# Kernel tuning notes

Measured on AMD Instinct MI355X. Metric: run time of the kernel, lower is better.

The kernel has to match this reference:

```python
import jax, jax.numpy as jnp
import numpy as np

N, M, K, D = 2048, 2048, 8, 64
BLUR, SCALING = 0.05, 0.8
EPS_MIN = BLUR ** 2            # geomloss: eps = blur^p, p=2
DIAM2 = 16.0                   # static diameter^2 estimate for jit-static eps schedule
NEG = -1e9                     # log-weight for masked-out points


def _eps_schedule():
    eps, e = [], DIAM2
    while e > EPS_MIN:
        eps.append(e)
        e *= SCALING ** 2      # geomloss multiplies eps by scaling^p per step
    eps.append(EPS_MIN)
    return jnp.asarray(eps, jnp.float32)


def _softmin(eps, C, h):
    # -eps * logsumexp_j( h_j - C_ij/eps );  C:[n,m], h:[m] (h = log_w + pot/eps)
    return -eps * jax.nn.logsumexp(h[None, :] - C / eps, axis=1)


def _sq_cost(u, v):
    # geomloss p=2 cost: ||u-v||^2 / 2
    d2 = jnp.sum(u * u, 1)[:, None] + jnp.sum(v * v, 1)[None, :] - 2.0 * (u @ v.T)
    return 0.5 * jnp.maximum(d2, 0.0)


def _sinkhorn_divergence(Cxy, Cxx, Cyy, log_a, log_b, a, b, eps_arr):
    # debiased sinkhorn divergence S = <a, f-f_aa> + <b, g-g_bb>, eps-scaling,
    # symmetric (averaged) updates; loop is detached, one differentiable
    # extrapolation step at eps_min (geomloss-style envelope gradient).
    Cxy_s, Cxx_s, Cyy_s = (jax.lax.stop_gradient(c) for c in (Cxy, Cxx, Cyy))
    n, m = Cxy.shape

    def step(carry, eps):
        f_ab, g_ab, f_aa, g_bb = carry
        ft = _softmin(eps, Cxy_s, log_b + g_ab / eps)
        gt = _softmin(eps, Cxy_s.T, log_a + f_ab / eps)
        f_aa = 0.5 * (f_aa + _softmin(eps, Cxx_s, log_a + f_aa / eps))
        g_bb = 0.5 * (g_bb + _softmin(eps, Cyy_s, log_b + g_bb / eps))
        return (0.5 * (f_ab + ft), 0.5 * (g_ab + gt), f_aa, g_bb), None

    init = (jnp.zeros(n, jnp.float32), jnp.zeros(m, jnp.float32),
            jnp.zeros(n, jnp.float32), jnp.zeros(m, jnp.float32))
    (f_ab, g_ab, f_aa, g_bb), _ = jax.lax.scan(step, init, eps_arr)
    f_ab, g_ab, f_aa, g_bb = (jax.lax.stop_gradient(p) for p in (f_ab, g_ab, f_aa, g_bb))

    eps = eps_arr[-1]
    f = _softmin(eps, Cxy, log_b + g_ab / eps)
    g = _softmin(eps, Cxy.T, log_a + f_ab / eps)
    faa = _softmin(eps, Cxx, log_a + f_aa / eps)
    gbb = _softmin(eps, Cyy, log_b + g_bb / eps)
    return jnp.sum(a * (f - faa)) + jnp.sum(b * (g - gbb))


def setup_inputs() -> dict:
    key = jax.random.key(0)
    k1, k2, k3, k4, k5 = jax.random.split(key, 5)
    return {
        "x": jax.random.normal(k1, (N, D), jnp.float32),
        "cluster_centers": jax.random.normal(k2, (K, D), jnp.float32),
        "filling_target": jax.random.uniform(k3, (K,), jnp.float32),
        "target": jax.random.normal(k4, (M, D), jnp.float32),
        "prediction": jax.random.randint(k5, (M,), 0, K, jnp.int64),
    }


def reference(x, cluster_centers, filling_target, target, prediction):
    # kmeans_predict: nearest center assignment
    d2c = jnp.sum((x[:, None, :] - cluster_centers[None, :, :]) ** 2, axis=-1)  # [N,K]
    pred_x = jnp.argmin(d2c, axis=1)                                            # [N]

    ks = jnp.arange(K)
    mx = (pred_x[None, :] == ks[:, None]).astype(jnp.float32)       # [K,N]
    my = (prediction[None, :] == ks[:, None]).astype(jnp.float32)   # [K,M]
    cnt_x, cnt_y = mx.sum(1), my.sum(1)

    # compute_cluster_filling_mse: cluster occupancy fraction vs target
    loss_fil = jnp.mean((cnt_x / N - filling_target) ** 2)

    a = mx / jnp.maximum(cnt_x, 1.0)[:, None]
    b = my / jnp.maximum(cnt_y, 1.0)[:, None]
    log_a = jnp.where(mx > 0, -jnp.log(jnp.maximum(cnt_x, 1.0))[:, None], NEG)
    log_b = jnp.where(my > 0, -jnp.log(jnp.maximum(cnt_y, 1.0))[:, None], NEG)
    valid = (cnt_x > 0.5) & (cnt_y > 0.5)

    # shared dense cost matrices (cluster structure enters only via weights)
    Cxy, Cxx, Cyy = _sq_cost(x, target), _sq_cost(x, x), _sq_cost(target, target)
    eps_arr = _eps_schedule()
    div = jax.vmap(lambda la, lb, aa, bb: _sinkhorn_divergence(
        Cxy, Cxx, Cyy, la, lb, aa, bb, eps_arr))(log_a, log_b, a, b)   # [K]

    loss_med = jnp.sum(jnp.where(valid, div, 0.0))
    return loss_fil + loss_med
```

## Files before the change

kernel.cpp:

```cpp
#include <hip/hip_runtime.h>

#define NN 2048
#define MM 2048
#define KC 8
#define DD 64
#define PN (NN + 4*KC + 32)
#define PM (MM + 4*KC + 32)
#define TOTROWS (2*(NN+MM))
#define CPAD (2*NN*MM + NN*NN + MM*MM + 6*(NN+MM) + 256)
#define PADV 3.0e38f
#define LN2F    0.6931471805599453f
#define INVLN2F 1.4426950408889634f

struct Params {
  const float* x; const float* centers; const float* ftarg;
  const float* y; const int* predy;
  float* out;
  int* zr;
  int* pred_x;
  int* cntx; int* cnty; int* off_x; int* off_y; int* pox; int* poy;
  int* bxy; int* byx; int* bxx; int* byy;
  int* tpre;
  float* la; float* lb; int* valid; float* acc;
  float* Xp; float* Yp; float* xn; float* yn;
  float* Fab; float* Faa; float* Gab; float* Gbb;
  int4* meta;
  float* fin;
  int* dsti;
  float* Call;
};

__device__ __forceinline__ float wredmax(float v){
  #pragma unroll
  for(int m=32;m>=1;m>>=1) v = fmaxf(v, __shfl_xor(v,m,64));
  return v;
}
__device__ __forceinline__ float wredsum(float v){
  #pragma unroll
  for(int m=32;m>=1;m>>=1) v += __shfl_xor(v,m,64);
  return v;
}

__global__ void __launch_bounds__(256) k_pred(Params p){
  const int gtid = blockIdx.x*blockDim.x + threadIdx.x;
  const int nth  = gridDim.x*blockDim.x;

  for(int i=gtid;i<2*PN;i+=nth){ p.Fab[i]=0.f; p.Faa[i]=0.f; }
  for(int j=gtid;j<2*PM;j+=nth){ p.Gab[j]=0.f; p.Gbb[j]=0.f; }

  for(int i=gtid;i<NN;i+=nth){
    const float4* xi = (const float4*)(p.x + i*DD);
    float best = 3.4e38f; int bk = 0;
    for(int k=0;k<KC;k++){
      const float4* ck = (const float4*)(p.centers + k*DD);
      float s = 0.f;
      #pragma unroll
      for(int q=0;q<DD/4;q++){ float4 a=xi[q], b=ck[q];
        float dx=a.x-b.x, dy=a.y-b.y, dz=a.z-b.z, dw=a.w-b.w;
        s += dx*dx+dy*dy+dz*dz+dw*dw; }
      if(s < best){ best = s; bk = k; }
    }
    p.pred_x[i] = bk;
    atomicAdd(&p.zr[8+bk], 1);
  }
  for(int j=gtid;j<MM;j+=nth) atomicAdd(&p.zr[16 + p.predy[j]], 1);
}

__global__ void __launch_bounds__(256) k_pack(Params p){
  __shared__ int scx[KC], scy[KC];
  __shared__ int sox[KC+1], soy[KC+1], spx[KC], spy[KC];
  __shared__ int sbxy[KC], sbyx[KC], sbxx[KC], sbyy[KC], sval[KC];
  __shared__ float sla[KC], slb[KC];
  const int tid = threadIdx.x;
  const int gtid = blockIdx.x*blockDim.x + tid;
  const int nth  = gridDim.x*blockDim.x;

  if(tid==0){
    int ox=0, oy=0, px=0, py=0; float lf=0.f;
    for(int k=0;k<KC;k++){
      int nk=p.zr[8+k], mk=p.zr[16+k];
      scx[k]=nk; scy[k]=mk;
      sox[k]=ox; soy[k]=oy; spx[k]=px; spy[k]=py;
      ox+=nk; oy+=mk; px=(px+nk+3)&~3; py=(py+mk+3)&~3;
      sla[k] = -logf(fmaxf((float)nk,1.f));
      slb[k] = -logf(fmaxf((float)mk,1.f));
      sval[k] = (nk>0 && mk>0)?1:0;
      float df = (float)nk/(float)NN - p.ftarg[k];
      lf += df*df;
    }
    sox[KC]=ox; soy[KC]=oy;
    int run=0;
    for(int k=0;k<KC;k++){ int nk=scx[k], mk=scy[k]; sbxy[k]=run; run+=nk*((mk+3)&~3); }
    for(int k=0;k<KC;k++){ int nk=scx[k], mk=scy[k]; sbyx[k]=run; run+=mk*((nk+3)&~3); }
    for(int k=0;k<KC;k++){ int nk=scx[k];            sbxx[k]=run; run+=nk*((nk+3)&~3); }
    for(int k=0;k<KC;k++){ int mk=scy[k];            sbyy[k]=run; run+=mk*((mk+3)&~3); }
    if(blockIdx.x==0){
      for(int k=0;k<KC;k++){
        p.cntx[k]=scx[k]; p.cnty[k]=scy[k];
        p.off_x[k]=sox[k]; p.off_y[k]=soy[k];
        p.pox[k]=spx[k]; p.poy[k]=spy[k];
        p.bxy[k]=sbxy[k]; p.byx[k]=sbyx[k]; p.bxx[k]=sbxx[k]; p.byy[k]=sbyy[k];
        p.la[k]=sla[k]; p.lb[k]=slb[k]; p.valid[k]=sval[k];
      }
      int trun=0;
      for(int e=0;e<32;e++){
        int seg=e>>3, k=e&7;
        int nk=scx[k], mk=scy[k];
        int nrows = (seg==0)?nk:(seg==1)?mk:(seg==2)?nk:mk;
        int rs    = (seg==0)?((mk+3)&~3):(seg==1)?((nk+3)&~3):(seg==2)?((nk+3)&~3):((mk+3)&~3);
        p.tpre[e]=trun;
        trun += ((nrows+63)>>6) * ((rs+63)>>6);
      }
      p.tpre[32]=trun;
      *p.acc = lf/(float)KC;
    }
  }
  __syncthreads();

  for(int i=gtid;i<NN;i+=nth){
    int k=p.pred_x[i];
    int pos = sox[k] + atomicAdd(&p.zr[24+k],1);
    const float4* xi=(const float4*)(p.x+i*DD);
    float4* dst=(float4*)(p.Xp+(size_t)pos*DD);
    float s=0.f;
    #pragma unroll
    for(int q=0;q<DD/4;q++){ float4 v=xi[q]; dst[q]=v;
      s += v.x*v.x+v.y*v.y+v.z*v.z+v.w*v.w; }
    p.xn[pos]=s;
  }
  for(int j=gtid;j<MM;j+=nth){
    int k=p.predy[j];
    int pos = soy[k] + atomicAdd(&p.zr[32+k],1);
    const float4* yj=(const float4*)(p.y+j*DD);
    float4* dst=(float4*)(p.Yp+(size_t)pos*DD);
    float s=0.f;
    #pragma unroll
    for(int q=0;q<DD/4;q++){ float4 v=yj[q]; dst[q]=v;
      s += v.x*v.x+v.y*v.y+v.z*v.z+v.w*v.w; }
    p.yn[pos]=s;
  }

  for(int row=gtid; row<TOTROWS; row+=nth){
    int grp = (row>=NN) + (row>=NN+MM) + (row>=2*NN+MM);
    int pidx = row - ((grp==0)?0:(grp==1)?NN:(grp==2)?(NN+MM):(2*NN+MM));
    const int* offs = (grp==0||grp==2)? sox : soy;
    int k=0;
    #pragma unroll
    for(int q=1;q<KC;q++) if(pidx>=offs[q]) k=q;
    int r = pidx - offs[k];
    int nk=scx[k], mk=scy[k];
    int rsx=(nk+3)&~3, rsy=(mk+3)&~3;
    int coff, rs, di; float hc, fv; int hoff;
    if(grp==0){ rs=rsy; coff=sbxy[k]+r*rs; hoff=spy[k]; hc=slb[k]; di=spx[k]+r;
      fv = sval[k] ?  1.f/(float)nk : 0.f; }
    else if(grp==1){ rs=rsx; coff=sbyx[k]+r*rs; hoff=spx[k]; hc=sla[k]; di=spy[k]+r;
      fv = sval[k] ?  1.f/(float)mk : 0.f; }
    else if(grp==2){ rs=rsx; coff=sbxx[k]+r*rs; hoff=spx[k]; hc=sla[k]; di=spx[k]+r;
      fv = sval[k] ? -1.f/(float)nk : 0.f; }
    else { rs=rsy; coff=sbyy[k]+r*rs; hoff=spy[k]; hc=slb[k]; di=spy[k]+r;
      fv = sval[k] ? -1.f/(float)mk : 0.f; }
    p.meta[row] = make_int4(coff, hoff, rs, __float_as_int(hc*INVLN2F));
    p.fin[row]  = fv;
    p.dsti[row] = di;
  }
}

__global__ void __launch_bounds__(256) k4_cost(Params p){
  __shared__ float As[64*68];
  __shared__ float Bt[64*68];
  const int tid = threadIdx.x;
  const int T = p.tpre[32];

  for(int tile=blockIdx.x; tile<T; tile+=gridDim.x){
    int e=0;
    for(int q=1;q<32;q++) if(tile>=p.tpre[q]) e=q;
    int seg=e>>3, k=e&7;
    int nk=p.cntx[k], mk=p.cnty[k];
    int rsx=(nk+3)&~3, rsy=(mk+3)&~3;
    const float *Apts, *Bpts, *nA, *nB; int nrows, ncol, rs, base;
    if(seg==0){ Apts=p.Xp+(size_t)p.off_x[k]*DD; Bpts=p.Yp+(size_t)p.off_y[k]*DD;
      nA=p.xn+p.off_x[k]; nB=p.yn+p.off_y[k]; nrows=nk; ncol=mk; rs=rsy; base=p.bxy[k]; }
    else if(seg==1){ Apts=p.Yp+(size_t)p.off_y[k]*DD; Bpts=p.Xp+(size_t)p.off_x[k]*DD;
      nA=p.yn+p.off_y[k]; nB=p.xn+p.off_x[k]; nrows=mk; ncol=nk; rs=rsx; base=p.byx[k]; }
    else if(seg==2){ Apts=p.Xp+(size_t)p.off_x[k]*DD; Bpts=Apts;
      nA=p.xn+p.off_x[k]; nB=nA; nrows=nk; ncol=nk; rs=rsx; base=p.bxx[k]; }
    else { Apts=p.Yp+(size_t)p.off_y[k]*DD; Bpts=Apts;
      nA=p.yn+p.off_y[k]; nB=nA; nrows=mk; ncol=mk; rs=rsy; base=p.byy[k]; }
    int ntc=(rs+63)>>6;
    int lt = tile - p.tpre[e];
    int tr = lt/ntc, tc = lt - tr*ntc;

    __syncthreads();
    for(int l=tid;l<1024;l+=256){
      int row=l>>4, c4=l&15;
      int gA=tr*64+row;
      float4 va = (gA<nrows)? ((const float4*)Apts)[gA*16+c4] : make_float4(0.f,0.f,0.f,0.f);
      *(float4*)&As[row*68 + c4*4] = va;
      int gB=tc*64+row;
      float4 vb = (gB<ncol)? ((const float4*)Bpts)[gB*16+c4] : make_float4(0.f,0.f,0.f,0.f);
      Bt[(c4*4+0)*68+row]=vb.x; Bt[(c4*4+1)*68+row]=vb.y;
      Bt[(c4*4+2)*68+row]=vb.z; Bt[(c4*4+3)*68+row]=vb.w;
    }
    __syncthreads();

    int tx=tid&15, ty=tid>>4;
    float4 acc[4] = {make_float4(0,0,0,0),make_float4(0,0,0,0),
                     make_float4(0,0,0,0),make_float4(0,0,0,0)};
    for(int kk=0;kk<64;kk+=4){
      float4 a0=*(float4*)&As[(ty*4+0)*68+kk];
      float4 a1=*(float4*)&As[(ty*4+1)*68+kk];
      float4 a2=*(float4*)&As[(ty*4+2)*68+kk];
      float4 a3=*(float4*)&As[(ty*4+3)*68+kk];
      float4 b0=*(float4*)&Bt[(kk+0)*68+tx*4];
      float4 b1=*(float4*)&Bt[(kk+1)*68+tx*4];
      float4 b2=*(float4*)&Bt[(kk+2)*68+tx*4];
      float4 b3=*(float4*)&Bt[(kk+3)*68+tx*4];
      #define ACCROW(i,AI) \
        acc[i].x = fmaf(AI.x,b0.x, fmaf(AI.y,b1.x, fmaf(AI.z,b2.x, fmaf(AI.w,b3.x, acc[i].x)))); \
        acc[i].y = fmaf(AI.x,b0.y, fmaf(AI.y,b1.y, fmaf(AI.z,b2.y, fmaf(AI.w,b3.y, acc[i].y)))); \
        acc[i].z = fmaf(AI.x,b0.z, fmaf(AI.y,b1.z, fmaf(AI.z,b2.z, fmaf(AI.w,b3.z, acc[i].z)))); \
        acc[i].w = fmaf(AI.x,b0.w, fmaf(AI.y,b1.w, fmaf(AI.w,b3.w, fmaf(AI.z,b2.w, acc[i].w))));
      ACCROW(0,a0) ACCROW(1,a1) ACCROW(2,a2) ACCROW(3,a3)
      #undef ACCROW
    }

    int gc0 = tc*64 + tx*4;
    #pragma unroll
    for(int i=0;i<4;i++){
      int gr = tr*64 + ty*4 + i;
      if(gr >= nrows) continue;
      float xr = nA[gr];
      float v[4]; float d[4]={acc[i].x,acc[i].y,acc[i].z,acc[i].w};
      #pragma unroll
      for(int j=0;j<4;j++){
        int gc = gc0+j;
        v[j] = PADV;
        if(gc < ncol) v[j] = 0.5f*fmaxf(xr + nB[gc] - 2.f*d[j], 0.f);
      }
      if(gc0+3 < rs){
        *(float4*)&p.Call[(size_t)base + (size_t)gr*rs + gc0] = make_float4(v[0],v[1],v[2],v[3]);
      } else {
        for(int j=0;j<4;j++) if(gc0+j < rs) p.Call[(size_t)base + (size_t)gr*rs + gc0+j] = v[j];
      }
    }
  }
}

__global__ void __launch_bounds__(256) k_iter(Params p, float eps, int cur){
  const int w = blockIdx.x*4 + (threadIdx.x>>6);
  const int lane = threadIdx.x & 63;
  const int r0 = w*2, r1 = r0+1;
  const int grp = (r0>=NN) + (r0>=NN+MM) + (r0>=2*NN+MM);
  const float* po; float* fam; int famN;
  if(grp==0){ po=p.Gab+cur*PM; fam=p.Fab; famN=PN; }
  else if(grp==1){ po=p.Fab+cur*PN; fam=p.Gab; famN=PM; }
  else if(grp==2){ po=p.Faa+cur*PN; fam=p.Faa; famN=PN; }
  else { po=p.Gbb+cur*PM; fam=p.Gbb; famN=PM; }

  int4 m0 = p.meta[r0], m1 = p.meta[r1];
  const float* C0=p.Call+m0.x; const float* P0=po+m0.y; float h0=__int_as_float(m0.w);
  const float* C1=p.Call+m1.x; const float* P1=po+m1.y; float h1=__int_as_float(m1.w);
  const int rs0=m0.z, rs1=m1.z, rsm = rs0>rs1?rs0:rs1;
  const float s1 = (1.0f/eps)*INVLN2F;

  float mA=-3.4e38f,sA=0.f,mB=-3.4e38f,sB=0.f;
  for(int c0=lane*4; c0<rsm; c0+=256){
    if(c0<rs0){
      float4 cv=*(const float4*)(C0+c0), pv=*(const float4*)(P0+c0);
      float w0=fmaf(pv.x-cv.x,s1,h0), w1=fmaf(pv.y-cv.y,s1,h0);
      float w2=fmaf(pv.z-cv.z,s1,h0), w3=fmaf(pv.w-cv.w,s1,h0);
      float lm=fmaxf(fmaxf(w0,w1),fmaxf(w2,w3));
      float mn=fmaxf(mA,lm);
      sA = sA*exp2f(mA-mn) + (exp2f(w0-mn)+exp2f(w1-mn)) + (exp2f(w2-mn)+exp2f(w3-mn));
      mA = mn;
    }
    if(c0<rs1){
      float4 cv=*(const float4*)(C1+c0), pv=*(const float4*)(P1+c0);
      float w0=fmaf(pv.x-cv.x,s1,h1), w1=fmaf(pv.y-cv.y,s1,h1);
      float w2=fmaf(pv.z-cv.z,s1,h1), w3=fmaf(pv.w-cv.w,s1,h1);
      float lm=fmaxf(fmaxf(w0,w1),fmaxf(w2,w3));
      float mn=fmaxf(mB,lm);
      sB = sB*exp2f(mB-mn) + (exp2f(w0-mn)+exp2f(w1-mn)) + (exp2f(w2-mn)+exp2f(w3-mn));
      mB = mn;
    }
  }
  float MA=wredmax(mA); float SA=wredsum(sA*exp2f(mA-MA));
  float MB=wredmax(mB); float SB=wredsum(sB*exp2f(mB-MB));
  float LA = -eps*LN2F*(MA + log2f(SA));
  float LB = -eps*LN2F*(MB + log2f(SB));

  if(lane==0){
    int d0=p.dsti[r0], d1=p.dsti[r1];
    fam[(1-cur)*famN+d0] = 0.5f*(fam[cur*famN+d0]+LA);
    fam[(1-cur)*famN+d1] = 0.5f*(fam[cur*famN+d1]+LB);
  }
}

__global__ void __launch_bounds__(256) k_final(Params p, float eps, int cur){
  __shared__ float bacc;
  if(threadIdx.x==0) bacc=0.f;
  __syncthreads();
  const int w = blockIdx.x*4 + (threadIdx.x>>6);
  const int lane = threadIdx.x & 63;
  const float s1 = (1.0f/eps)*INVLN2F;

  #pragma unroll
  for(int hh=0; hh<2; ++hh){
    int row = w*2 + hh;
    float fv = p.fin[row];
    if(fv == 0.f) continue;
    int grp = (row>=NN) + (row>=NN+MM) + (row>=2*NN+MM);
    const float* po = (grp==0)?(p.Gab+cur*PM):(grp==1)?(p.Fab+cur*PN)
                     :(grp==2)?(p.Faa+cur*PN):(p.Gbb+cur*PM);
    int4 mt = p.meta[row];
    const float* Cb=p.Call+mt.x; const float* Pv=po+mt.y; float hb=__int_as_float(mt.w);
    float m=-3.4e38f, s=0.f;
    for(int c0=lane*4; c0<mt.z; c0+=256){
      float4 cv=*(const float4*)(Cb+c0), pv=*(const float4*)(Pv+c0);
      float w0=fmaf(pv.x-cv.x,s1,hb), w1=fmaf(pv.y-cv.y,s1,hb);
      float w2=fmaf(pv.z-cv.z,s1,hb), w3=fmaf(pv.w-cv.w,s1,hb);
      float lm=fmaxf(fmaxf(w0,w1),fmaxf(w2,w3));
      float mn=fmaxf(m,lm);
      s = s*exp2f(m-mn) + (exp2f(w0-mn)+exp2f(w1-mn)) + (exp2f(w2-mn)+exp2f(w3-mn));
      m = mn;
    }
    float M=wredmax(m); float S=wredsum(s*exp2f(m-M));
    float L = -eps*LN2F*(M + log2f(S));
    if(lane==0) atomicAdd(&bacc, L*fv);
  }
  __syncthreads();
  if(threadIdx.x==0){
    if(bacc != 0.f) atomicAdd(p.acc, bacc);
    __threadfence();
    int prev = __hip_atomic_fetch_add(p.zr, 1, __ATOMIC_ACQ_REL, __HIP_MEMORY_SCOPE_AGENT);
    if(prev == (int)gridDim.x-1){
      __threadfence();
      p.out[0] = __hip_atomic_load(p.acc, __ATOMIC_RELAXED, __HIP_MEMORY_SCOPE_AGENT);
    }
  }
}

extern "C" void kernel_launch(void* const* d_in, const int* in_sizes, int n_in,
                              void* d_out, int out_size, void* d_ws, size_t ws_size,
                              hipStream_t stream)
{
  Params p;
  p.x       = (const float*)d_in[0];
  p.centers = (const float*)d_in[1];
  p.ftarg   = (const float*)d_in[2];
  p.y       = (const float*)d_in[3];
  p.predy   = (const int*)d_in[4];
  p.out     = (float*)d_out;

  char* w = (char*)d_ws; size_t o = 0;
  auto A = [&](size_t bytes)->char*{ char* r = w + o; o = (o + bytes + 255) & ~(size_t)255; return r; };
  p.zr   =(int*)A(64*4);
  p.pred_x=(int*)A(NN*4);
  p.cntx =(int*)A(KC*4); p.cnty=(int*)A(KC*4);
  p.off_x=(int*)A(KC*4); p.off_y=(int*)A(KC*4);
  p.pox  =(int*)A(KC*4); p.poy =(int*)A(KC*4);
  p.bxy  =(int*)A(KC*4); p.byx =(int*)A(KC*4);
  p.bxx  =(int*)A(KC*4); p.byy =(int*)A(KC*4);
  p.tpre =(int*)A(33*4);
  p.la=(float*)A(KC*4); p.lb=(float*)A(KC*4); p.valid=(int*)A(KC*4);
  p.acc=(float*)A(4);
  p.Xp=(float*)A((size_t)NN*DD*4); p.Yp=(float*)A((size_t)MM*DD*4);
  p.xn=(float*)A(NN*4); p.yn=(float*)A(MM*4);
  p.Fab=(float*)A((size_t)2*PN*4); p.Faa=(float*)A((size_t)2*PN*4);
  p.Gab=(float*)A((size_t)2*PM*4); p.Gbb=(float*)A((size_t)2*PM*4);
  p.meta=(int4*)A((size_t)TOTROWS*16);
  p.fin =(float*)A((size_t)TOTROWS*4);
  p.dsti=(int*)A((size_t)TOTROWS*4);
  p.Call=(float*)A((size_t)CPAD*4);

  hipMemsetAsync(p.zr, 0, 64*4, stream);
  hipLaunchKernelGGL(k_pred,  dim3(16),   dim3(256), 0, stream, p);
  hipLaunchKernelGGL(k_pack,  dim3(32),   dim3(256), 0, stream, p);
  hipLaunchKernelGGL(k4_cost, dim3(1024), dim3(256), 0, stream, p);

  const double EMIN = 0.05*0.05, S2 = 0.8*0.8;
  float epsv[40]; int ne = 0;
  { double e = 16.0; while(e > EMIN){ epsv[ne++] = (float)e; e *= S2; } epsv[ne++] = (float)EMIN; }

  for(int it=0; it<ne; ++it)
    hipLaunchKernelGGL(k_iter, dim3(TOTROWS/8), dim3(256), 0, stream, p, epsv[it], it&1);

  hipLaunchKernelGGL(k_final, dim3(TOTROWS/8), dim3(256), 0, stream, p, (float)EMIN, ne&1);
}
```

Before: 309.9 us.

## Process four rows per wave in Sinkhorn iterations and reduce final sum deterministically

Each wavefront in k_iter and k_final now handles four softmin rows instead of two, which halves the grid and gives each lane more independent loads and exp work in flight. The final kernel no longer uses shared and global atomics with a last-block counter. It writes per-block partial sums, and a new single-block kernel adds them up, costing one extra launch. The rows in a wave have different lengths, so unequal rows leave more lanes idle, and using fewer blocks may lower occupancy.

Result: slower. 325.6 us (+5.1%).

```diff
diff --git a/kernel.cpp b/kernel.cpp
--- a/kernel.cpp
+++ b/kernel.cpp
@@ -11,6 +11,7 @@
 #define PADV 3.0e38f
 #define LN2F    0.6931471805599453f
 #define INVLN2F 1.4426950408889634f
+#define NBLK (TOTROWS/16)
 
 struct Params {
   const float* x; const float* centers; const float* ftarg;
@@ -22,6 +23,7 @@
   int* bxy; int* byx; int* bxx; int* byy;
   int* tpre;
   float* la; float* lb; int* valid; float* acc;
+  float* part;
   float* Xp; float* Yp; float* xn; float* yn;
   float* Fab; float* Faa; float* Gab; float* Gbb;
   int4* meta;
@@ -219,7 +221,7 @@
         acc[i].x = fmaf(AI.x,b0.x, fmaf(AI.y,b1.x, fmaf(AI.z,b2.x, fmaf(AI.w,b3.x, acc[i].x)))); \
         acc[i].y = fmaf(AI.x,b0.y, fmaf(AI.y,b1.y, fmaf(AI.z,b2.y, fmaf(AI.w,b3.y, acc[i].y)))); \
         acc[i].z = fmaf(AI.x,b0.z, fmaf(AI.y,b1.z, fmaf(AI.z,b2.z, fmaf(AI.w,b3.z, acc[i].z)))); \
-        acc[i].w = fmaf(AI.x,b0.w, fmaf(AI.y,b1.w, fmaf(AI.w,b3.w, fmaf(AI.z,b2.w, acc[i].w))));
+        acc[i].w = fmaf(AI.x,b0.w, fmaf(AI.y,b1.w, fmaf(AI.z,b2.w, fmaf(AI.w,b3.w, acc[i].w))));
       ACCROW(0,a0) ACCROW(1,a1) ACCROW(2,a2) ACCROW(3,a3)
       #undef ACCROW
     }
@@ -246,10 +248,19 @@
   }
 }
 
+#define LSE_STEP(Ci,Pi,hi,mi,si) { \
+  float4 cv=*(const float4*)(Ci+c0), pv=*(const float4*)(Pi+c0); \
+  float w0=fmaf(pv.x-cv.x,s1,hi), w1=fmaf(pv.y-cv.y,s1,hi); \
+  float w2=fmaf(pv.z-cv.z,s1,hi), w3=fmaf(pv.w-cv.w,s1,hi); \
+  float lm=fmaxf(fmaxf(w0,w1),fmaxf(w2,w3)); \
+  float mn=fmaxf(mi,lm); \
+  si = si*exp2f(mi-mn) + (exp2f(w0-mn)+exp2f(w1-mn)) + (exp2f(w2-mn)+exp2f(w3-mn)); \
+  mi = mn; }
+
 __global__ void __launch_bounds__(256) k_iter(Params p, float eps, int cur){
   const int w = blockIdx.x*4 + (threadIdx.x>>6);
   const int lane = threadIdx.x & 63;
-  const int r0 = w*2, r1 = r0+1;
+  const int r0 = w*4;
   const int grp = (r0>=NN) + (r0>=NN+MM) + (r0>=2*NN+MM);
   const float* po; float* fam; int famN;
   if(grp==0){ po=p.Gab+cur*PM; fam=p.Fab; famN=PN; }
@@ -257,87 +268,98 @@
   else if(grp==2){ po=p.Faa+cur*PN; fam=p.Faa; famN=PN; }
   else { po=p.Gbb+cur*PM; fam=p.Gbb; famN=PM; }
 
-  int4 m0 = p.meta[r0], m1 = p.meta[r1];
-  const float* C0=p.Call+m0.x; const float* P0=po+m0.y; float h0=__int_as_float(m0.w);
-  const float* C1=p.Call+m1.x; const float* P1=po+m1.y; float h1=__int_as_float(m1.w);
-  const int rs0=m0.z, rs1=m1.z, rsm = rs0>rs1?rs0:rs1;
+  int4 m0=p.meta[r0], m1=p.meta[r0+1], m2=p.meta[r0+2], m3=p.meta[r0+3];
+  const float *C0=p.Call+m0.x, *C1=p.Call+m1.x, *C2=p.Call+m2.x, *C3=p.Call+m3.x;
+  const float *P0=po+m0.y, *P1=po+m1.y, *P2=po+m2.y, *P3=po+m3.y;
+  float h0=__int_as_float(m0.w), h1=__int_as_float(m1.w);
+  float h2=__int_as_float(m2.w), h3=__int_as_float(m3.w);
+  const int rs0=m0.z, rs1=m1.z, rs2=m2.z, rs3=m3.z;
+  int rsm = rs0>rs1?rs0:rs1; if(rs2>rsm) rsm=rs2; if(rs3>rsm) rsm=rs3;
   const float s1 = (1.0f/eps)*INVLN2F;
 
   float mA=-3.4e38f,sA=0.f,mB=-3.4e38f,sB=0.f;
+  float mC=-3.4e38f,sC=0.f,mD=-3.4e38f,sD=0.f;
   for(int c0=lane*4; c0<rsm; c0+=256){
-    if(c0<rs0){
-      float4 cv=*(const float4*)(C0+c0), pv=*(const float4*)(P0+c0);
-      float w0=fmaf(pv.x-cv.x,s1,h0), w1=fmaf(pv.y-cv.y,s1,h0);
-      float w2=fmaf(pv.z-cv.z,s1,h0), w3=fmaf(pv.w-cv.w,s1,h0);
-      float lm=fmaxf(fmaxf(w0,w1),fmaxf(w2,w3));
-      float mn=fmaxf(mA,lm);
-      sA = sA*exp2f(mA-mn) + (exp2f(w0-mn)+exp2f(w1-mn)) + (exp2f(w2-mn)+exp2f(w3-mn));
-      mA = mn;
-    }
-    if(c0<rs1){
-      float4 cv=*(const float4*)(C1+c0), pv=*(const float4*)(P1+c0);
-      float w0=fmaf(pv.x-cv.x,s1,h1), w1=fmaf(pv.y-cv.y,s1,h1);
-      float w2=fmaf(pv.z-cv.z,s1,h1), w3=fmaf(pv.w-cv.w,s1,h1);
-      float lm=fmaxf(fmaxf(w0,w1),fmaxf(w2,w3));
-      float mn=fmaxf(mB,lm);
-      sB = sB*exp2f(mB-mn) + (exp2f(w0-mn)+exp2f(w1-mn)) + (exp2f(w2-mn)+exp2f(w3-mn));
-      mB = mn;
-    }
+    if(c0<rs0) LSE_STEP(C0,P0,h0,mA,sA)
+    if(c0<rs1) LSE_STEP(C1,P1,h1,mB,sB)
+    if(c0<rs2) LSE_STEP(C2,P2,h2,mC,sC)
+    if(c0<rs3) LSE_STEP(C3,P3,h3,mD,sD)
   }
   float MA=wredmax(mA); float SA=wredsum(sA*exp2f(mA-MA));
   float MB=wredmax(mB); float SB=wredsum(sB*exp2f(mB-MB));
-  float LA = -eps*LN2F*(MA + log2f(SA));
-  float LB = -eps*LN2F*(MB + log2f(SB));
+  float MC=wredmax(mC); float SC=wredsum(sC*exp2f(mC-MC));
+  float MD=wredmax(mD); float SD=wredsum(sD*exp2f(mD-MD));
 
   if(lane==0){
-    int d0=p.dsti[r0], d1=p.dsti[r1];
-    fam[(1-cur)*famN+d0] = 0.5f*(fam[cur*famN+d0]+LA);
-    fam[(1-cur)*famN+d1] = 0.5f*(fam[cur*famN+d1]+LB);
+    float LA = -eps*LN2F*(MA + log2f(SA));
+    float LB = -eps*LN2F*(MB + log2f(SB));
+    float LC = -eps*LN2F*(MC + log2f(SC));
+    float LD = -eps*LN2F*(MD + log2f(SD));
+    int d0=p.dsti[r0], d1=p.dsti[r0+1], d2=p.dsti[r0+2], d3=p.dsti[r0+3];
+    float* fn = fam + (1-cur)*famN;
+    const float* fo = fam + cur*famN;
+    fn[d0] = 0.5f*(fo[d0]+LA);
+    fn[d1] = 0.5f*(fo[d1]+LB);
+    fn[d2] = 0.5f*(fo[d2]+LC);
+    fn[d3] = 0.5f*(fo[d3]+LD);
   }
 }
 
 __global__ void __launch_bounds__(256) k_final(Params p, float eps, int cur){
-  __shared__ float bacc;
-  if(threadIdx.x==0) bacc=0.f;
-  __syncthreads();
+  __shared__ float sp[4];
   const int w = blockIdx.x*4 + (threadIdx.x>>6);
   const int lane = threadIdx.x & 63;
+  const int wv = threadIdx.x>>6;
+  const int r0 = w*4;
+  const int grp = (r0>=NN) + (r0>=NN+MM) + (r0>=2*NN+MM);
+  const float* po = (grp==0)?(p.Gab+cur*PM):(grp==1)?(p.Fab+cur*PN)
+                   :(grp==2)?(p.Faa+cur*PN):(p.Gbb+cur*PM);
+
+  int4 m0=p.meta[r0], m1=p.meta[r0+1], m2=p.meta[r0+2], m3=p.meta[r0+3];
+  float fv0=p.fin[r0], fv1=p.fin[r0+1], fv2=p.fin[r0+2], fv3=p.fin[r0+3];
+  const float *C0=p.Call+m0.x, *C1=p.Call+m1.x, *C2=p.Call+m2.x, *C3=p.Call+m3.x;
+  const float *P0=po+m0.y, *P1=po+m1.y, *P2=po+m2.y, *P3=po+m3.y;
+  float h0=__int_as_float(m0.w), h1=__int_as_float(m1.w);
+  float h2=__int_as_float(m2.w), h3=__int_as_float(m3.w);
+  const int rs0=m0.z, rs1=m1.z, rs2=m2.z, rs3=m3.z;
+  int rsm = rs0>rs1?rs0:rs1; if(rs2>rsm) rsm=rs2; if(rs3>rsm) rsm=rs3;
   const float s1 = (1.0f/eps)*INVLN2F;
 
-  #pragma unroll
-  for(int hh=0; hh<2; ++hh){
-    int row = w*2 + hh;
-    float fv = p.fin[row];
-    if(fv == 0.f) continue;
-    int grp = (row>=NN) + (row>=NN+MM) + (row>=2*NN+MM);
-    const float* po = (grp==0)?(p.Gab+cur*PM):(grp==1)?(p.Fab+cur*PN)
-                     :(grp==2)?(p.Faa+cur*PN):(p.Gbb+cur*PM);
-    int4 mt = p.meta[row];
-    const float* Cb=p.Call+mt.x; const float* Pv=po+mt.y; float hb=__int_as_float(mt.w);
-    float m=-3.4e38f, s=0.f;
-    for(int c0=lane*4; c0<mt.z; c0+=256){
-      float4 cv=*(const float4*)(Cb+c0), pv=*(const float4*)(Pv+c0);
-      float w0=fmaf(pv.x-cv.x,s1,hb), w1=fmaf(pv.y-cv.y,s1,hb);
-      float w2=fmaf(pv.z-cv.z,s1,hb), w3=fmaf(pv.w-cv.w,s1,hb);
-      float lm=fmaxf(fmaxf(w0,w1),fmaxf(w2,w3));
-      float mn=fmaxf(m,lm);
-      s = s*exp2f(m-mn) + (exp2f(w0-mn)+exp2f(w1-mn)) + (exp2f(w2-mn)+exp2f(w3-mn));
-      m = mn;
-    }
-    float M=wredmax(m); float S=wredsum(s*exp2f(m-M));
-    float L = -eps*LN2F*(M + log2f(S));
-    if(lane==0) atomicAdd(&bacc, L*fv);
+  float mA=-3.4e38f,sA=0.f,mB=-3.4e38f,sB=0.f;
+  float mC=-3.4e38f,sC=0.f,mD=-3.4e38f,sD=0.f;
+  for(int c0=lane*4; c0<rsm; c0+=256){
+    if(c0<rs0) LSE_STEP(C0,P0,h0,mA,sA)
+    if(c0<rs1) LSE_STEP(C1,P1,h1,mB,sB)
+    if(c0<rs2) LSE_STEP(C2,P2,h2,mC,sC)
+    if(c0<rs3) LSE_STEP(C3,P3,h3,mD,sD)
+  }
+  float MA=wredmax(mA); float SA=wredsum(sA*exp2f(mA-MA));
+  float MB=wredmax(mB); float SB=wredsum(sB*exp2f(mB-MB));
+  float MC=wredmax(mC); float SC=wredsum(sC*exp2f(mC-MC));
+  float MD=wredmax(mD); float SD=wredsum(sD*exp2f(mD-MD));
+
+  if(lane==0){
+    float part = 0.f;
+    if(fv0!=0.f) part += fv0 * (-eps*LN2F*(MA + log2f(SA)));
+    if(fv1!=0.f) part += fv1 * (-eps*LN2F*(MB + log2f(SB)));
+    if(fv2!=0.f) part += fv2 * (-eps*LN2F*(MC + log2f(SC)));
+    if(fv3!=0.f) part += fv3 * (-eps*LN2F*(MD + log2f(SD)));
+    sp[wv] = part;
   }
   __syncthreads();
-  if(threadIdx.x==0){
-    if(bacc != 0.f) atomicAdd(p.acc, bacc);
-    __threadfence();
-    int prev = __hip_atomic_fetch_add(p.zr, 1, __ATOMIC_ACQ_REL, __HIP_MEMORY_SCOPE_AGENT);
-    if(prev == (int)gridDim.x-1){
-      __threadfence();
-      p.out[0] = __hip_atomic_load(p.acc, __ATOMIC_RELAXED, __HIP_MEMORY_SCOPE_AGENT);
-    }
-  }
+  if(threadIdx.x==0)
+    p.part[blockIdx.x] = sp[0]+sp[1]+sp[2]+sp[3];
+}
+
+__global__ void __launch_bounds__(256) k_out(Params p){
+  __shared__ float red[4];
+  float s=0.f;
+  for(int i=threadIdx.x;i<NBLK;i+=256) s += p.part[i];
+  s = wredsum(s);
+  if((threadIdx.x&63)==0) red[threadIdx.x>>6]=s;
+  __syncthreads();
+  if(threadIdx.x==0)
+    p.out[0] = red[0]+red[1]+red[2]+red[3] + *p.acc;
 }
 
 extern "C" void kernel_launch(void* const* d_in, const int* in_sizes, int n_in,
@@ -364,6 +386,7 @@
   p.tpre =(int*)A(33*4);
   p.la=(float*)A(KC*4); p.lb=(float*)A(KC*4); p.valid=(int*)A(KC*4);
   p.acc=(float*)A(4);
+  p.part=(float*)A(NBLK*4);
   p.Xp=(float*)A((size_t)NN*DD*4); p.Yp=(float*)A((size_t)MM*DD*4);
   p.xn=(float*)A(NN*4); p.yn=(float*)A(MM*4);
   p.Fab=(float*)A((size_t)2*PN*4); p.Faa=(float*)A((size_t)2*PN*4);
@@ -383,7 +406,8 @@
   { double e = 16.0; while(e > EMIN){ epsv[ne++] = (float)e; e *= S2; } epsv[ne++] = (float)EMIN; }
 
   for(int it=0; it<ne; ++it)
-    hipLaunchKernelGGL(k_iter, dim3(TOTROWS/8), dim3(256), 0, stream, p, epsv[it], it&1);
-
-  hipLaunchKernelGGL(k_final, dim3(TOTROWS/8), dim3(256), 0, stream, p, (float)EMIN, ne&1);
-}
+    hipLaunchKernelGGL(k_iter, dim3(NBLK), dim3(256), 0, stream, p, epsv[it], it&1);
+
+  hipLaunchKernelGGL(k_final, dim3(NBLK), dim3(256), 0, stream, p, (float)EMIN, ne&1);
+  hipLaunchKernelGGL(k_out,   dim3(1),    dim3(256), 0, stream, p);
+}
```
